# Kernel optimization log

Measured on AMD Instinct MI355X. Metric: run time of the kernel, lower is better.

## Reference

```python
import jax, jax.numpy as jnp
import numpy as np

# Model dims (match init_kwargs)
E = 16            # real experts
Z = 16            # zero experts (identity)
TOP_K = 4
H = 1024          # hidden_size
I = 512           # intermediate_size per expert
T = 4096          # tokens
ROUTED_SCALING = 1.0


def setup_inputs() -> dict:
    key = jax.random.key(0)
    ks = jax.random.split(key, 6)
    s_h = 1.0 / np.sqrt(H)
    s_i = 1.0 / np.sqrt(I)
    return {
        "hidden_states": jax.random.normal(ks[0], (T, H), jnp.float32),
        # router over E + Z total slots (real experts + zero experts)
        "router_weight": jax.random.normal(ks[1], (E + Z, H), jnp.float32) * s_h,
        "e_score_bias": jax.random.normal(ks[2], (E + Z,), jnp.float32) * 0.01,
        # SwiGLU expert weights
        "w_gate": jax.random.normal(ks[3], (E, H, I), jnp.float32) * s_h,
        "w_up": jax.random.normal(ks[4], (E, H, I), jnp.float32) * s_h,
        "w_down": jax.random.normal(ks[5], (E, I, H), jnp.float32) * s_i,
    }


def reference(hidden_states, router_weight, e_score_bias, w_gate, w_up, w_down):
    x = hidden_states  # [T, H]
    # --- Router (float32, router_dtype == 'float32') ---
    logits = jnp.einsum("th,eh->te", x.astype(jnp.float32), router_weight)  # [T, E+Z]
    scores = jax.nn.softmax(logits, axis=-1)
    # top-k selected on bias-corrected scores; weights taken from raw scores,
    # renormalize=False
    _, topk_ids = jax.lax.top_k(scores + e_score_bias[None, :], TOP_K)  # [T, k]
    topk_w = jnp.take_along_axis(scores, topk_ids, axis=-1)             # [T, k]
    # --- Dispatch/combine weights over all E+Z slots ---
    onehot = jax.nn.one_hot(topk_ids, E + Z, dtype=jnp.float32)  # [T, k, E+Z]
    combine = jnp.einsum("tk,tks->ts", topk_w, onehot)           # [T, E+Z]
    cw_real = combine[:, :E].astype(x.dtype)      # [T, E] routed-expert weights
    zero_w = combine[:, E:].sum(-1).astype(x.dtype)  # [T] identity weight sum
    # --- Grouped-expert SwiGLU (dense dispatch reference) ---
    g = jnp.einsum("th,ehi->eti", x, w_gate)   # [E, T, I]
    u = jnp.einsum("th,ehi->eti", x, w_up)     # [E, T, I]
    act = jax.nn.silu(g) * u
    eout = jnp.einsum("eti,eih->eth", act, w_down)  # [E, T, H]
    routed = jnp.einsum("eth,te->th", eout, cw_real)  # [T, H]
    # zero experts: identity contribution (zero_expert_type == 'identity')
    out = routed * ROUTED_SCALING + zero_w[:, None] * x
    return out
```

## Files before the change

kernel.cpp:

```cpp
#include <hip/hip_runtime.h>
#include <stdint.h>

#define T_TOK 4096
#define Hd    1024
#define Id    512
#define NE    16
#define NSLOT 32
#define TOPK  4
#define ECAP  1024
#define MAXT  (NE * (ECAP/128))

typedef __bf16 bf16x8 __attribute__((ext_vector_type(8)));
typedef float  floatx4 __attribute__((ext_vector_type(4)));

#define WAIT_VM(n) asm volatile("s_waitcnt vmcnt(" #n ")" ::: "memory")

static __device__ __forceinline__ void wg_barrier(){
  asm volatile("" ::: "memory");
  __builtin_amdgcn_s_barrier();
  asm volatile("" ::: "memory");
}

static __device__ __forceinline__ unsigned short f2bf(float f){
  unsigned int u = __float_as_uint(f);
  u = u + 0x7fffu + ((u >> 16) & 1u);
  return (unsigned short)(u >> 16);
}

static __device__ __forceinline__ uint32_t bfpack(uint32_t hi_src, uint32_t lo_src){
  return __builtin_amdgcn_perm(hi_src, lo_src, 0x07060302u);
}

static __device__ __forceinline__ void load_lds16(const void* g, void* l){
  __builtin_amdgcn_global_load_lds((const __attribute__((address_space(1))) void*)g,
                                   (__attribute__((address_space(3))) void*)l, 16, 0, 0);
}

__global__ __launch_bounds__(256) void router_kernel(
    const float* __restrict__ x, const float* __restrict__ rw,
    unsigned short* __restrict__ xb, float* __restrict__ logits,
    int* __restrict__ cursors){
  const int tid = threadIdx.x;
  if (blockIdx.x == 0 && tid < NE) cursors[tid] = 0;
  const int lane = tid & 63, wid = tid >> 6;
  const int t = blockIdx.x * 4 + wid;
  const int l4 = lane * 4;
  const float* xr = x + (size_t)t * Hd;
  unsigned short* xo = xb + (size_t)t * Hd;
  float acc[NSLOT];
  #pragma unroll
  for (int s = 0; s < NSLOT; ++s) acc[s] = 0.f;
  #pragma unroll
  for (int c = 0; c < 4; ++c){
    const int h = c * 256 + l4;
    float4 xv = *(const float4*)(xr + h);
    ushort4 o;
    o.x = f2bf(xv.x); o.y = f2bf(xv.y); o.z = f2bf(xv.z); o.w = f2bf(xv.w);
    *(ushort4*)(xo + h) = o;
    #pragma unroll
    for (int s = 0; s < NSLOT; ++s){
      float4 rv = *(const float4*)(rw + (size_t)s * Hd + h);
      acc[s] += xv.x*rv.x + xv.y*rv.y + xv.z*rv.z + xv.w*rv.w;
    }
  }
  #pragma unroll
  for (int s = 0; s < NSLOT; ++s){
    float v = acc[s];
    v += __shfl_xor(v, 32);
    v += __shfl_xor(v, 16);
    v += __shfl_xor(v, 8);
    v += __shfl_xor(v, 4);
    v += __shfl_xor(v, 2);
    v += __shfl_xor(v, 1);
    acc[s] = v;
  }
  if (lane == 0){
    float* lp = logits + (size_t)t * NSLOT;
    #pragma unroll
    for (int s = 0; s < NSLOT; s += 4){
      float4 o; o.x = acc[s]; o.y = acc[s+1]; o.z = acc[s+2]; o.w = acc[s+3];
      *(float4*)(lp + s) = o;
    }
  }
}

__global__ __launch_bounds__(256) void transpose_kernel(
    const float* __restrict__ wg, const float* __restrict__ wu,
    const float* __restrict__ wd,
    unsigned short* __restrict__ wgb, unsigned short* __restrict__ wub,
    unsigned short* __restrict__ wdb){
  const int tb = blockIdx.x;
  const int tid = threadIdx.x;
  const float* src; unsigned short* dst; int R, C, rt, ct;
  const int arr = tb >> 11;
  const int rem = tb & 2047;
  const int e  = rem >> 7;
  const int t2 = rem & 127;
  if (arr == 0)      { src = wg; dst = wgb; R = Hd; C = Id; rt = t2 >> 3; ct = t2 & 7;  }
  else if (arr == 1) { src = wu; dst = wub; R = Hd; C = Id; rt = t2 >> 3; ct = t2 & 7;  }
  else               { src = wd; dst = wdb; R = Id; C = Hd; rt = t2 >> 4; ct = t2 & 15; }
  const int r0 = rt * 64, c0 = ct * 64;
  const float* s = src + (size_t)e * R * C;
  unsigned short* d = dst + (size_t)e * R * C;
  const int r_idx = tid >> 4;
  const int c_idx = tid & 15;
  const int rr = r0 + r_idx * 4;
  const int cc = c0 + c_idx * 4;
  uint4 u0 = *(const uint4*)(s + (size_t)(rr + 0)*C + cc);
  uint4 u1 = *(const uint4*)(s + (size_t)(rr + 1)*C + cc);
  uint4 u2 = *(const uint4*)(s + (size_t)(rr + 2)*C + cc);
  uint4 u3 = *(const uint4*)(s + (size_t)(rr + 3)*C + cc);
  uint2 o;
  o.x = bfpack(u1.x, u0.x); o.y = bfpack(u3.x, u2.x);
  *(uint2*)(d + (size_t)(cc + 0)*R + rr) = o;
  o.x = bfpack(u1.y, u0.y); o.y = bfpack(u3.y, u2.y);
  *(uint2*)(d + (size_t)(cc + 1)*R + rr) = o;
  o.x = bfpack(u1.z, u0.z); o.y = bfpack(u3.z, u2.z);
  *(uint2*)(d + (size_t)(cc + 2)*R + rr) = o;
  o.x = bfpack(u1.w, u0.w); o.y = bfpack(u3.w, u2.w);
  *(uint2*)(d + (size_t)(cc + 3)*R + rr) = o;
}

__global__ __launch_bounds__(256) void topk_kernel(
    const float* __restrict__ logits, const float* __restrict__ bias,
    const float* __restrict__ x,
    int* __restrict__ cursors, int* __restrict__ rowmap, float* __restrict__ roww,
    float* __restrict__ out){
  __shared__ float szw[8];
  const int tid = threadIdx.x;
  if (tid < 8){
    const int t = blockIdx.x * 8 + tid;
    float sc[32], bsc[32];
    #pragma unroll
    for (int i = 0; i < 32; i += 4){
      float4 v = *(const float4*)(logits + (size_t)t*NSLOT + i);
      sc[i] = v.x; sc[i+1] = v.y; sc[i+2] = v.z; sc[i+3] = v.w;
    }
    float mx = sc[0];
    #pragma unroll
    for (int i = 1; i < 32; ++i) mx = fmaxf(mx, sc[i]);
    float sum = 0.f;
    #pragma unroll
    for (int i = 0; i < 32; ++i){ sc[i] = __expf(sc[i]-mx); sum += sc[i]; }
    float inv = 1.f / sum;
    #pragma unroll
    for (int i = 0; i < 32; ++i){ sc[i] *= inv; bsc[i] = sc[i] + bias[i]; }
    unsigned int chosen = 0;
    float zw = 0.f;
    #pragma unroll
    for (int k = 0; k < TOPK; ++k){
      float bv = -1e30f, bw = 0.f; int best = 0;
      #pragma unroll
      for (int i = 0; i < 32; ++i){
        float v = ((chosen >> i) & 1u) ? -1e30f : bsc[i];
        if (v > bv){ bv = v; best = i; bw = sc[i]; }
      }
      chosen |= (1u << best);
      if (best < NE){
        int pos = atomicAdd(&cursors[best], 1);
        rowmap[best*ECAP + pos] = t;
        roww[best*ECAP + pos]   = bw;
      } else zw += bw;
    }
    szw[tid] = zw;
  }
  __syncthreads();
  const int lane = tid & 63, wid = tid >> 6;
  const size_t base = (size_t)blockIdx.x * 8 * Hd;
  #pragma unroll
  for (int r0 = 0; r0 < 8; r0 += 4){
    int r = r0 + wid;
    float s = szw[r];
    const float4* xs = (const float4*)(x + base + (size_t)r*Hd);
    float4* os = (float4*)(out + base + (size_t)r*Hd);
    #pragma unroll
    for (int q = 0; q < 4; ++q){
      float4 v = xs[lane + q*64];
      float4 o; o.x = v.x*s; o.y = v.y*s; o.z = v.z*s; o.w = v.w*s;
      os[lane + q*64] = o;
    }
  }
}

static __device__ __forceinline__ bool tile_map(const int* __restrict__ counts, int tile,
                                                int& e, int& off, int& ne, int& m0){
  int cumT = 0; e = -1; ne = 0; m0 = 0;
  #pragma unroll
  for (int ee = 0; ee < NE; ++ee){
    int c = counts[ee];
    int nt = (c + 127) >> 7;
    bool here = (e < 0) && (tile < cumT + nt);
    if (here){ e = ee; ne = c; m0 = (tile - cumT) * 128; }
    cumT += nt;
  }
  off = (e >= 0) ? e * ECAP : 0;
  return e >= 0;
}

__global__ __launch_bounds__(256, 2) void gateup_kernel(
    const unsigned short* __restrict__ xb,
    const unsigned short* __restrict__ wgb,
    const unsigned short* __restrict__ wub,
    const int* __restrict__ counts,
    const int* __restrict__ rowmap,
    const float* __restrict__ roww,
    unsigned short* __restrict__ act){
  const int b = blockIdx.x;
  int e, off, ne, m0;
  if (!tile_map(counts, b >> 2, e, off, ne, m0)) return;
  const int n0 = (b & 3) * 128;

  __shared__ unsigned short sA [2][128*32];
  __shared__ unsigned short sBg[2][128*32];
  __shared__ unsigned short sBu[2][128*32];
  __shared__ int sT[128];

  const int tid = threadIdx.x, lane = tid & 63, wid = tid >> 6;
  if (tid < 128){ int r = m0 + tid; sT[tid] = rowmap[off + ((r < ne) ? r : 0)]; }
  __syncthreads();

  const int r_in = lane >> 2, seg = lane & 3;
  const int rt0 = wid*32 + r_in, rt1 = rt0 + 16;
  const size_t wbase = (size_t)e * Id * Hd;

  const unsigned short* pA0 = xb + (size_t)sT[rt0]*Hd + seg*8;
  const unsigned short* pA1 = xb + (size_t)sT[rt1]*Hd + seg*8;
  const unsigned short* pG0 = wgb + wbase + (size_t)(n0+rt0)*Hd + seg*8;
  const unsigned short* pG1 = wgb + wbase + (size_t)(n0+rt1)*Hd + seg*8;
  const unsigned short* pU0 = wub + wbase + (size_t)(n0+rt0)*Hd + seg*8;
  const unsigned short* pU1 = wub + wbase + (size_t)(n0+rt1)*Hd + seg*8;
  const int dA0 = wid*1024, dA1 = wid*1024 + 512;

  floatx4 accg[4][4], accu[4][4];
  #pragma unroll
  for (int i = 0; i < 4; ++i)
    #pragma unroll
    for (int j = 0; j < 4; ++j){
      floatx4 z = {0.f,0.f,0.f,0.f};
      accg[i][j] = z; accu[i][j] = z;
    }
  const int wm = (wid & 1) * 64, wn = (wid >> 1) * 64;
  const int fm = lane & 15, fq = lane >> 4;

  load_lds16(pA0, &sA[0][dA0]);  load_lds16(pA1, &sA[0][dA1]);
  load_lds16(pG0, &sBg[0][dA0]); load_lds16(pG1, &sBg[0][dA1]);
  load_lds16(pU0, &sBu[0][dA0]); load_lds16(pU1, &sBu[0][dA1]);

  #pragma unroll 2
  for (int kit = 0; kit < 32; ++kit){
    const int cur = kit & 1;
    if (kit < 31){
      const int nk = (kit+1)*32;
      const int nb = 1 - cur;
      load_lds16(pA0 + nk, &sA[nb][dA0]);  load_lds16(pA1 + nk, &sA[nb][dA1]);
      load_lds16(pG0 + nk, &sBg[nb][dA0]); load_lds16(pG1 + nk, &sBg[nb][dA1]);
      load_lds16(pU0 + nk, &sBu[nb][dA0]); load_lds16(pU1 + nk, &sBu[nb][dA1]);
      WAIT_VM(6);
    } else {
      WAIT_VM(0);
    }
    wg_barrier();
    bf16x8 av[4], bgv[4], buv[4];
    #pragma unroll
    for (int i = 0; i < 4; ++i)
      av[i] = *(const bf16x8*)(&sA[cur][(wm + i*16 + fm)*32 + fq*8]);
    #pragma unroll
    for (int j = 0; j < 4; ++j){
      bgv[j] = *(const bf16x8*)(&sBg[cur][(wn + j*16 + fm)*32 + fq*8]);
      buv[j] = *(const bf16x8*)(&sBu[cur][(wn + j*16 + fm)*32 + fq*8]);
    }
    #pragma unroll
    for (int i = 0; i < 4; ++i)
      #pragma unroll
      for (int j = 0; j < 4; ++j){
        accg[i][j] = __builtin_amdgcn_mfma_f32_16x16x32_bf16(av[i], bgv[j], accg[i][j], 0, 0, 0);
        accu[i][j] = __builtin_amdgcn_mfma_f32_16x16x32_bf16(av[i], buv[j], accu[i][j], 0, 0, 0);
      }
    wg_barrier();
  }

  #pragma unroll
  for (int i = 0; i < 4; ++i){
    #pragma unroll
    for (int r = 0; r < 4; ++r){
      int row = wm + i*16 + fq*4 + r;
      if (m0 + row < ne){
        float w = roww[off + m0 + row];
        size_t rb = (size_t)(off + m0 + row) * Id + n0;
        #pragma unroll
        for (int j = 0; j < 4; ++j){
          float g = accg[i][j][r];
          float u = accu[i][j][r];
          float a = (g / (1.f + __expf(-g))) * u * w;
          act[rb + wn + j*16 + fm] = f2bf(a);
        }
      }
    }
  }
}

__global__ __launch_bounds__(256, 4) void down_kernel(
    const unsigned short* __restrict__ act,
    const unsigned short* __restrict__ wdb,
    const int* __restrict__ counts,
    const int* __restrict__ rowmap,
    float* __restrict__ out){
  const int b = blockIdx.x;
  int e, off, ne, m0;
  if (!tile_map(counts, b >> 3, e, off, ne, m0)) return;
  const int n0 = (b & 7) * 128;

  __shared__ unsigned short sA[2][128*32];
  __shared__ unsigned short sB[2][128*32];
  __shared__ int sT[128];

  const int tid = threadIdx.x, lane = tid & 63, wid = tid >> 6;
  if (tid < 128){ int r = m0 + tid; sT[tid] = (r < ne) ? rowmap[off + r] : 0; }

  const int r_in = lane >> 2, seg = lane & 3;
  const int rt0 = wid*32 + r_in, rt1 = rt0 + 16;
  const int gr0 = off + ((m0 + rt0 < ne) ? (m0 + rt0) : 0);
  const int gr1 = off + ((m0 + rt1 < ne) ? (m0 + rt1) : 0);
  const size_t wbase = (size_t)e * Hd * Id;
  const unsigned short* pA0 = act + (size_t)gr0*Id + seg*8;
  const unsigned short* pA1 = act + (size_t)gr1*Id + seg*8;
  const unsigned short* pB0 = wdb + wbase + (size_t)(n0+rt0)*Id + seg*8;
  const unsigned short* pB1 = wdb + wbase + (size_t)(n0+rt1)*Id + seg*8;
  const int dA0 = wid*1024, dA1 = wid*1024 + 512;

  floatx4 acc[4][4];
  #pragma unroll
  for (int i = 0; i < 4; ++i)
    #pragma unroll
    for (int j = 0; j < 4; ++j){ floatx4 z = {0.f,0.f,0.f,0.f}; acc[i][j] = z; }
  const int wm = (wid & 1) * 64, wn = (wid >> 1) * 64;
  const int fm = lane & 15, fq = lane >> 4;

  load_lds16(pA0, &sA[0][dA0]); load_lds16(pA1, &sA[0][dA1]);
  load_lds16(pB0, &sB[0][dA0]); load_lds16(pB1, &sB[0][dA1]);

  #pragma unroll 2
  for (int kit = 0; kit < 16; ++kit){
    const int cur = kit & 1;
    if (kit < 15){
      const int nk = (kit+1)*32;
      const int nb = 1 - cur;
      load_lds16(pA0 + nk, &sA[nb][dA0]); load_lds16(pA1 + nk, &sA[nb][dA1]);
      load_lds16(pB0 + nk, &sB[nb][dA0]); load_lds16(pB1 + nk, &sB[nb][dA1]);
      WAIT_VM(4);
    } else {
      WAIT_VM(0);
    }
    wg_barrier();
    bf16x8 av[4], bv[4];
    #pragma unroll
    for (int i = 0; i < 4; ++i) av[i] = *(const bf16x8*)(&sA[cur][(wm + i*16 + fm)*32 + fq*8]);
    #pragma unroll
    for (int j = 0; j < 4; ++j) bv[j] = *(const bf16x8*)(&sB[cur][(wn + j*16 + fm)*32 + fq*8]);
    #pragma unroll
    for (int i = 0; i < 4; ++i)
      #pragma unroll
      for (int j = 0; j < 4; ++j)
        acc[i][j] = __builtin_amdgcn_mfma_f32_16x16x32_bf16(av[i], bv[j], acc[i][j], 0, 0, 0);
    wg_barrier();
  }

  #pragma unroll
  for (int i = 0; i < 4; ++i){
    #pragma unroll
    for (int r = 0; r < 4; ++r){
      int row = wm + i*16 + fq*4 + r;
      if (m0 + row < ne){
        int t = sT[row];
        #pragma unroll
        for (int j = 0; j < 4; ++j)
          atomicAdd(&out[(size_t)t*Hd + n0 + wn + j*16 + fm], acc[i][j][r]);
      }
    }
  }
}

extern "C" void kernel_launch(void* const* d_in, const int* in_sizes, int n_in,
                              void* d_out, int out_size, void* d_ws, size_t ws_size,
                              hipStream_t stream){
  (void)in_sizes; (void)n_in; (void)out_size; (void)ws_size;
  const float* x    = (const float*)d_in[0];
  const float* rw   = (const float*)d_in[1];
  const float* bias = (const float*)d_in[2];
  const float* wg   = (const float*)d_in[3];
  const float* wu   = (const float*)d_in[4];
  const float* wd   = (const float*)d_in[5];
  float* out = (float*)d_out;

  char* ws = (char*)d_ws;
  const size_t WSZ = (size_t)NE * Id * Hd * 2;
  unsigned short* wgb = (unsigned short*)(ws);
  unsigned short* wub = (unsigned short*)(ws + WSZ);
  unsigned short* wdb = (unsigned short*)(ws + 2*WSZ);
  unsigned short* xb  = (unsigned short*)(ws + 3*WSZ);
  unsigned short* act = (unsigned short*)(ws + 3*WSZ + (size_t)T_TOK*Hd*2);
  char* misc = ws + 3*WSZ + (size_t)T_TOK*Hd*2 + (size_t)NE*ECAP*Id*2;

  const size_t LOGB = (size_t)T_TOK * NSLOT * 4;
  float* logits  = (float*)misc;
  int*   cursors = (int*)(misc + LOGB);
  char* p2 = misc + LOGB + 256;
  int*   rowmap = (int*)p2;                     p2 += (size_t)NE*ECAP*4;
  float* roww   = (float*)p2;

  router_kernel<<<T_TOK/4, 256, 0, stream>>>(x, rw, xb, logits, cursors);
  transpose_kernel<<<6144, 256, 0, stream>>>(wg, wu, wd, wgb, wub, wdb);
  topk_kernel<<<T_TOK/8, 256, 0, stream>>>(logits, bias, x, cursors, rowmap, roww, out);
  gateup_kernel<<<MAXT*4, 256, 0, stream>>>(xb, wgb, wub, cursors, rowmap, roww, act);
  down_kernel<<<MAXT*8, 256, 0, stream>>>(act, wdb, cursors, rowmap, out);
}
```

Measured before the change: 321.9 us.

## Tile router over 8 tokens x 8 slots per wave with transposed shuffle reduction

The router kernel now has each block handle 8 tokens, with each wave computing 8 router slots for all 8 tokens. Each router-weight load is reused across 8 tokens instead of every wave reloading all 32 slot rows. The per-slot butterfly reductions are replaced by a transpose-style shuffle reduction, so each lane ends up holding one token-slot logit and all lanes write. The cost is that each wave now reloads the 8 token rows of x, and the 64-float accumulator raises register pressure.

```diff
diff --git a/kernel.cpp b/kernel.cpp
--- a/kernel.cpp
+++ b/kernel.cpp
@@ -42,46 +42,50 @@
     int* __restrict__ cursors){
   const int tid = threadIdx.x;
   if (blockIdx.x == 0 && tid < NE) cursors[tid] = 0;
-  const int lane = tid & 63, wid = tid >> 6;
-  const int t = blockIdx.x * 4 + wid;
+  const int lane = tid & 63, sg = tid >> 6;
+  const int t0 = blockIdx.x * 8;
   const int l4 = lane * 4;
-  const float* xr = x + (size_t)t * Hd;
-  unsigned short* xo = xb + (size_t)t * Hd;
-  float acc[NSLOT];
-  #pragma unroll
-  for (int s = 0; s < NSLOT; ++s) acc[s] = 0.f;
+
+  float v[64];
+  #pragma unroll
+  for (int i = 0; i < 64; ++i) v[i] = 0.f;
+
   #pragma unroll
   for (int c = 0; c < 4; ++c){
     const int h = c * 256 + l4;
-    float4 xv = *(const float4*)(xr + h);
-    ushort4 o;
-    o.x = f2bf(xv.x); o.y = f2bf(xv.y); o.z = f2bf(xv.z); o.w = f2bf(xv.w);
-    *(ushort4*)(xo + h) = o;
-    #pragma unroll
-    for (int s = 0; s < NSLOT; ++s){
-      float4 rv = *(const float4*)(rw + (size_t)s * Hd + h);
-      acc[s] += xv.x*rv.x + xv.y*rv.y + xv.z*rv.z + xv.w*rv.w;
-    }
-  }
-  #pragma unroll
-  for (int s = 0; s < NSLOT; ++s){
-    float v = acc[s];
-    v += __shfl_xor(v, 32);
-    v += __shfl_xor(v, 16);
-    v += __shfl_xor(v, 8);
-    v += __shfl_xor(v, 4);
-    v += __shfl_xor(v, 2);
-    v += __shfl_xor(v, 1);
-    acc[s] = v;
-  }
-  if (lane == 0){
-    float* lp = logits + (size_t)t * NSLOT;
-    #pragma unroll
-    for (int s = 0; s < NSLOT; s += 4){
-      float4 o; o.x = acc[s]; o.y = acc[s+1]; o.z = acc[s+2]; o.w = acc[s+3];
-      *(float4*)(lp + s) = o;
-    }
-  }
+    float4 xv[8];
+    #pragma unroll
+    for (int t = 0; t < 8; ++t)
+      xv[t] = *(const float4*)(x + (size_t)(t0 + t) * Hd + h);
+    if (sg == 0){
+      #pragma unroll
+      for (int t = 0; t < 8; ++t){
+        ushort4 o;
+        o.x = f2bf(xv[t].x); o.y = f2bf(xv[t].y);
+        o.z = f2bf(xv[t].z); o.w = f2bf(xv[t].w);
+        *(ushort4*)(xb + (size_t)(t0 + t) * Hd + h) = o;
+      }
+    }
+    #pragma unroll
+    for (int s = 0; s < 8; ++s){
+      float4 rv = *(const float4*)(rw + (size_t)(sg * 8 + s) * Hd + h);
+      #pragma unroll
+      for (int t = 0; t < 8; ++t)
+        v[t*8 + s] += xv[t].x*rv.x + xv[t].y*rv.y + xv[t].z*rv.z + xv[t].w*rv.w;
+    }
+  }
+
+  #pragma unroll
+  for (int off = 1; off < 64; off <<= 1){
+    #pragma unroll
+    for (int i = 0; i < 64; i += 2*off){
+      const int j = i + off;
+      float send  = (lane & off) ? v[i] : v[j];
+      float other = __shfl_xor(send, off);
+      v[i] = ((lane & off) ? v[j] : v[i]) + other;
+    }
+  }
+  logits[(size_t)(t0 + (lane >> 3)) * NSLOT + sg * 8 + (lane & 7)] = v[0];
 }
 
 __global__ __launch_bounds__(256) void transpose_kernel(
@@ -408,7 +412,7 @@
   int*   rowmap = (int*)p2;                     p2 += (size_t)NE*ECAP*4;
   float* roww   = (float*)p2;
 
-  router_kernel<<<T_TOK/4, 256, 0, stream>>>(x, rw, xb, logits, cursors);
+  router_kernel<<<T_TOK/8, 256, 0, stream>>>(x, rw, xb, logits, cursors);
   transpose_kernel<<<6144, 256, 0, stream>>>(wg, wu, wd, wgb, wub, wdb);
   topk_kernel<<<T_TOK/8, 256, 0, stream>>>(logits, bias, x, cursors, rowmap, roww, out);
   gateup_kernel<<<MAXT*4, 256, 0, stream>>>(xb, wgb, wub, cursors, rowmap, roww, act);
```

Result: faster. 282.1 us (-12.4%).
